# Kernel tuning notes

Hardware: AMD Instinct MI355X
Metric: run time of the kernel (lower is better)

The kernel has to match this reference:

```python
import jax, jax.numpy as jnp
import numpy as np

N_POINTS, N_TYPES, PER_TYPE, HIST, IN_U, U = 32768, 4, 8192, 32, 128, 128

def setup_inputs() -> dict:
    key = jax.random.key(0)
    ks = jax.random.split(key, 8)
    return {
        "current_node_state": jax.random.normal(ks[0], (N_POINTS, IN_U), jnp.float32),
        "historical_buffer": jax.random.normal(ks[1], (N_POINTS, HIST, U), jnp.float32),
        "entity_idx": jax.random.randint(ks[2], (N_TYPES, PER_TYPE), 0, N_POINTS, jnp.int32),
        "q_w": jax.random.normal(ks[3], (N_TYPES, IN_U, U), jnp.float32),
        "k_w": jax.random.normal(ks[4], (N_TYPES, U, U), jnp.float32),
        "v_w": jax.random.normal(ks[5], (N_TYPES, U, U), jnp.float32),
        "fc_w": jax.random.normal(ks[6], (N_TYPES, U, U), jnp.float32),
    }

def reference(current_node_state, historical_buffer, entity_idx, q_w, k_w, v_w, fc_w):
    # Batched-by-type gather (the original Python loop over entity types,
    # vectorized since all types have equal counts here).
    x = current_node_state[entity_idx]        # (T, N, IN_U)
    h = historical_buffer[entity_idx]         # (T, N, H, U)
    q = jnp.einsum('tne,teu->tnu', x, q_w)[:, :, None, :]   # (T, N, 1, U)
    k = jnp.einsum('tnhu,tuv->tnhv', h, k_w)                # (T, N, H, U)
    v = jnp.einsum('tnhu,tuv->tnhv', h, v_w)                # (T, N, H, U)
    raw = jnp.einsum('tnou,tnhu->tnoh', q, k)               # (T, N, 1, H)
    # NOTE: original uses F.softmax(raw_score) with implicit dim; for a 3D
    # tensor torch's legacy rule picks dim=0 (the per-type entity axis).
    attn = jax.nn.softmax(raw, axis=1)                      # softmax over N within each type
    agg = jnp.einsum('tnoh,tnhu->tnou', attn, v)            # (T, N, 1, U)
    out = jax.nn.relu(jnp.einsum('tnou,tuv->tnov', agg, fc_w)) + q
    # cat over types along node dim, then final squeeze -> (n_points, U)
    return out.reshape(N_TYPES * PER_TYPE, U)
```

## Files before the change

### kernel.cpp

```cpp
#include <hip/hip_runtime.h>
#include <math.h>

#define NPTS 32768
#define NTYPES 4
#define PER_TYPE 8192
#define HIST 32
#define UD 128
#define XT_STRIDE 68


__device__ __forceinline__ unsigned fkey(float x) {
    unsigned b = __float_as_uint(x);
    return (b & 0x80000000u) ? ~b : (b | 0x80000000u);
}
__device__ __forceinline__ float funkey(unsigned k) {
    unsigned b = (k & 0x80000000u) ? (k & 0x7fffffffu) : ~k;
    return __uint_as_float(b);
}

__global__ __launch_bounds__(128) void prep_kernel(
    const float* __restrict__ k_w, const float* __restrict__ v_w,
    const float* __restrict__ fc_w, float* __restrict__ kT,
    float* __restrict__ wvf, unsigned* __restrict__ Mbits, float* __restrict__ S)
{
    int r = blockIdx.x;
    int t = blockIdx.y;
    int u = threadIdx.x;
    kT[(t * UD + r) * UD + u] = k_w[(t * UD + u) * UD + r];
    float acc = 0.f;
    const float* vrow = v_w + (t * UD + r) * UD;
    const float* fb = fc_w + t * UD * UD;
    #pragma unroll 8
    for (int m = 0; m < UD; ++m)
        acc = fmaf(vrow[m], fb[m * UD + u], acc);
    wvf[(t * UD + r) * UD + u] = acc;
    if (r == 0 && t == 0) { Mbits[u] = 0u; S[u] = 0.f; }
}

__global__ __launch_bounds__(256) void qqk_kernel(
    const float* __restrict__ x, const int* __restrict__ idx,
    const float* __restrict__ q_w, const float* __restrict__ kT,
    float* __restrict__ q_out, float* __restrict__ qk_out)
{
    __shared__ float xT[UD * XT_STRIDE];
    __shared__ float qT[UD * XT_STRIDE];
    __shared__ int srow[64];
    int tx = threadIdx.x;
    int bn = blockIdx.x;
    int t  = blockIdx.y;
    int n0 = bn * 64;

    if (tx < 64) srow[tx] = idx[t * PER_TYPE + n0 + tx];
    __syncthreads();

    {
        int e = tx & 127;
        int half = tx >> 7;
        for (int i = 0; i < 32; ++i) {
            int ent = half * 32 + i;
            xT[e * XT_STRIDE + ent] = x[(size_t)srow[ent] * UD + e];
        }
    }
    __syncthreads();

    const int c4 = (tx & 31) * 4;
    const int eg = tx >> 5;
    float acc[8][4];

    #pragma unroll
    for (int i = 0; i < 8; ++i)
        #pragma unroll
        for (int j = 0; j < 4; ++j) acc[i][j] = 0.f;
    {
        const float* qw = q_w + t * UD * UD;
        for (int e = 0; e < UD; ++e) {
            float4 w = *(const float4*)(qw + e * UD + c4);
            const float* xr = &xT[e * XT_STRIDE + eg * 8];
            float4 a0 = *(const float4*)(xr);
            float4 a1 = *(const float4*)(xr + 4);
            float av[8] = {a0.x, a0.y, a0.z, a0.w, a1.x, a1.y, a1.z, a1.w};
            #pragma unroll
            for (int i = 0; i < 8; ++i) {
                acc[i][0] = fmaf(av[i], w.x, acc[i][0]);
                acc[i][1] = fmaf(av[i], w.y, acc[i][1]);
                acc[i][2] = fmaf(av[i], w.z, acc[i][2]);
                acc[i][3] = fmaf(av[i], w.w, acc[i][3]);
            }
        }
    }
    #pragma unroll
    for (int i = 0; i < 8; ++i) {
        int g = t * PER_TYPE + n0 + eg * 8 + i;
        *(float4*)(q_out + (size_t)g * UD + c4) =
            make_float4(acc[i][0], acc[i][1], acc[i][2], acc[i][3]);
    }
    #pragma unroll
    for (int j = 0; j < 4; ++j) {
        float4 lo = make_float4(acc[0][j], acc[1][j], acc[2][j], acc[3][j]);
        float4 hi = make_float4(acc[4][j], acc[5][j], acc[6][j], acc[7][j]);
        *(float4*)(&qT[(c4 + j) * XT_STRIDE + eg * 8]) = lo;
        *(float4*)(&qT[(c4 + j) * XT_STRIDE + eg * 8 + 4]) = hi;
    }
    __syncthreads();

    #pragma unroll
    for (int i = 0; i < 8; ++i)
        #pragma unroll
        for (int j = 0; j < 4; ++j) acc[i][j] = 0.f;
    {
        const float* kw = kT + t * UD * UD;
        for (int v = 0; v < UD; ++v) {
            float4 w = *(const float4*)(kw + v * UD + c4);
            const float* qr = &qT[v * XT_STRIDE + eg * 8];
            float4 a0 = *(const float4*)(qr);
            float4 a1 = *(const float4*)(qr + 4);
            float av[8] = {a0.x, a0.y, a0.z, a0.w, a1.x, a1.y, a1.z, a1.w};
            #pragma unroll
            for (int i = 0; i < 8; ++i) {
                acc[i][0] = fmaf(av[i], w.x, acc[i][0]);
                acc[i][1] = fmaf(av[i], w.y, acc[i][1]);
                acc[i][2] = fmaf(av[i], w.z, acc[i][2]);
                acc[i][3] = fmaf(av[i], w.w, acc[i][3]);
            }
        }
    }
    #pragma unroll
    for (int i = 0; i < 8; ++i) {
        int g = t * PER_TYPE + n0 + eg * 8 + i;
        *(float4*)(qk_out + (size_t)g * UD + c4) =
            make_float4(acc[i][0], acc[i][1], acc[i][2], acc[i][3]);
    }
}

__global__ __launch_bounds__(256) void raw_kernel(
    const float* __restrict__ hist, const int* __restrict__ idx,
    const float* __restrict__ qk, float* __restrict__ raw,
    unsigned* __restrict__ Mbits)
{
    __shared__ int srow[32];
    int tx = threadIdx.x;
    int bn = blockIdx.x;
    int t  = blockIdx.y;
    int n0 = bn * 32;
    if (tx < 32) srow[tx] = idx[t * PER_TYPE + n0 + tx];
    __syncthreads();
    int sub = tx & 7;
    int hh  = tx >> 3;
    float vmax = -INFINITY;
    for (int ei = 0; ei < 32; ++ei) {
        int g = t * PER_TYPE + n0 + ei;
        const float* qr = qk + (size_t)g * UD + sub * 16;
        float4 q0 = *(const float4*)(qr);
        float4 q1 = *(const float4*)(qr + 4);
        float4 q2 = *(const float4*)(qr + 8);
        float4 q3 = *(const float4*)(qr + 12);
        const float* hr = hist + ((size_t)srow[ei] * HIST + hh) * UD + sub * 16;
        float4 h0 = *(const float4*)(hr);
        float4 h1 = *(const float4*)(hr + 4);
        float4 h2 = *(const float4*)(hr + 8);
        float4 h3 = *(const float4*)(hr + 12);
        float a = q0.x * h0.x + q0.y * h0.y + q0.z * h0.z + q0.w * h0.w;
        a = fmaf(q1.x, h1.x, fmaf(q1.y, h1.y, fmaf(q1.z, h1.z, fmaf(q1.w, h1.w, a))));
        a = fmaf(q2.x, h2.x, fmaf(q2.y, h2.y, fmaf(q2.z, h2.z, fmaf(q2.w, h2.w, a))));
        a = fmaf(q3.x, h3.x, fmaf(q3.y, h3.y, fmaf(q3.z, h3.z, fmaf(q3.w, h3.w, a))));
        a += __shfl_xor(a, 1);
        a += __shfl_xor(a, 2);
        a += __shfl_xor(a, 4);
        vmax = fmaxf(vmax, a);
        if (sub == 0) raw[(size_t)g * HIST + hh] = a;
    }
    if (sub == 0) atomicMax(&Mbits[t * HIST + hh], fkey(vmax));
}

__global__ __launch_bounds__(256) void sum_kernel(
    const float* __restrict__ raw, const unsigned* __restrict__ Mbits,
    float* __restrict__ S)
{
    __shared__ float red[8][32];
    int tx = threadIdx.x;
    int c = blockIdx.x;
    int t = blockIdx.y;
    int hh = tx & 31;
    int nsl = tx >> 5;
    float M = funkey(Mbits[t * HIST + hh]);
    float s = 0.f;
    for (int i = 0; i < 32; ++i) {
        int n = c * 256 + i * 8 + nsl;
        float r = raw[((size_t)t * PER_TYPE + n) * HIST + hh];
        float e = r - M;
        if (e > -85.f) s += expf(e);
    }
    red[nsl][hh] = s;
    __syncthreads();
    if (tx < 32) {
        float tot = 0.f;
        #pragma unroll
        for (int k = 0; k < 8; ++k) tot += red[k][tx];
        atomicAdd(&S[t * HIST + tx], tot);
    }
}

__global__ __launch_bounds__(256) void out_kernel(
    const float* __restrict__ hist, const int* __restrict__ idx,
    const float* __restrict__ q, const float* __restrict__ raw,
    const unsigned* __restrict__ Mbits, const float* __restrict__ S,
    const float* __restrict__ wvf, float* __restrict__ out)
{
    __shared__ float shbar[4][UD];
    int tx = threadIdx.x;
    int wave = tx >> 6;
    int lane = tx & 63;
    int g = blockIdx.x * 4 + wave;
    int t = g >> 13;
    float w = 0.f;
    if (lane < 32) {
        float r = raw[(size_t)g * HIST + lane];
        float M = funkey(Mbits[t * HIST + lane]);
        float e = r - M;
        if (e > -75.f) w = expf(e) / S[t * HIST + lane];
    }
    unsigned long long act = __ballot(w != 0.f);
    int u2 = lane * 2;
    float2 qv = *(const float2*)(q + (size_t)g * UD + u2);
    float2 o;
    if (act == 0ull) {
        o = qv;
    } else {
        int row = idx[g];
        float2 hb = make_float2(0.f, 0.f);
        unsigned long long m = act;
        while (m) {
            int hh = __ffsll(m) - 1;
            m &= m - 1;
            float wv = __shfl(w, hh);
            float2 hv = *(const float2*)(hist + ((size_t)row * HIST + hh) * UD + u2);
            hb.x = fmaf(wv, hv.x, hb.x);
            hb.y = fmaf(wv, hv.y, hb.y);
        }
        shbar[wave][u2] = hb.x;
        shbar[wave][u2 + 1] = hb.y;
        float2 a = make_float2(0.f, 0.f);
        const float* wt = wvf + t * UD * UD;
        for (int e = 0; e < UD; ++e) {
            float hbe = shbar[wave][e];
            float2 wr = *(const float2*)(wt + e * UD + u2);
            a.x = fmaf(hbe, wr.x, a.x);
            a.y = fmaf(hbe, wr.y, a.y);
        }
        o.x = fmaxf(a.x, 0.f) + qv.x;
        o.y = fmaxf(a.y, 0.f) + qv.y;
    }
    *(float2*)(out + (size_t)g * UD + u2) = o;
}

extern "C" void kernel_launch(void* const* d_in, const int* in_sizes, int n_in,
                              void* d_out, int out_size, void* d_ws, size_t ws_size,
                              hipStream_t stream) {
    const float* x    = (const float*)d_in[0];
    const float* hist = (const float*)d_in[1];
    const int*   idx  = (const int*)d_in[2];
    const float* q_w  = (const float*)d_in[3];
    const float* k_w  = (const float*)d_in[4];
    const float* v_w  = (const float*)d_in[5];
    const float* fc_w = (const float*)d_in[6];
    float* out = (float*)d_out;

    float* ws = (float*)d_ws;
    float* q     = ws;
    float* qk    = ws + 4194304;
    float* raw   = ws + 8388608;
    unsigned* Mb = (unsigned*)(ws + 9437184);
    float* S     = ws + 9437312;
    float* kT    = ws + 9437440;
    float* wvf   = ws + 9502976;

    prep_kernel<<<dim3(128, 4), 128, 0, stream>>>(k_w, v_w, fc_w, kT, wvf, Mb, S);
    qqk_kernel<<<dim3(128, 4), 256, 0, stream>>>(x, idx, q_w, kT, q, qk);
    raw_kernel<<<dim3(256, 4), 256, 0, stream>>>(hist, idx, qk, raw, Mb);
    sum_kernel<<<dim3(32, 4), 256, 0, stream>>>(raw, Mb, S);
    out_kernel<<<8192, 256, 0, stream>>>(hist, idx, q, raw, Mb, S, wvf, out);
}
```

Measured before the change: 747.9 us.

## Restructure raw_kernel: stage qk in LDS, wider per-thread loads, block-level max

Raw-score kernel now handles 16 entities per block (twice as many blocks) and stages each entity's qk row in shared memory instead of re-reading it from global memory per thread group. Each thread covers 32 elements of the history row with 8 float4 loads and uses four independent partial sums, which needs one fewer shuffle step. The per-column max is reduced in shared memory before one global atomic per column per block, cutting global atomic traffic. The cost is extra LDS use, more registers per thread and a second block barrier.

```diff
diff --git a/kernel.cpp b/kernel.cpp
--- a/kernel.cpp
+++ b/kernel.cpp
@@ -137,39 +137,68 @@
     const float* __restrict__ qk, float* __restrict__ raw,
     unsigned* __restrict__ Mbits)
 {
-    __shared__ int srow[32];
+    __shared__ int srow[16];
+    __shared__ float sqk[16 * UD];
+    __shared__ unsigned smax[HIST];
     int tx = threadIdx.x;
     int bn = blockIdx.x;
     int t  = blockIdx.y;
-    int n0 = bn * 32;
-    if (tx < 32) srow[tx] = idx[t * PER_TYPE + n0 + tx];
-    __syncthreads();
-    int sub = tx & 7;
-    int hh  = tx >> 3;
+    int n0 = bn * 16;
+    if (tx < 16) srow[tx] = idx[t * PER_TYPE + n0 + tx];
+    if (tx < HIST) smax[tx] = 0u;
+    {
+        int e = tx >> 4;
+        int c = (tx & 15) * 8;
+        const float* src = qk + ((size_t)(t * PER_TYPE + n0 + e)) * UD + c;
+        float4 a = *(const float4*)(src);
+        float4 b = *(const float4*)(src + 4);
+        *(float4*)(&sqk[e * UD + c]) = a;
+        *(float4*)(&sqk[e * UD + c + 4]) = b;
+    }
+    __syncthreads();
+
+    int sub = tx & 3;
+    int hh  = (tx >> 2) & 31;
+    int eh  = tx >> 7;
     float vmax = -INFINITY;
-    for (int ei = 0; ei < 32; ++ei) {
-        int g = t * PER_TYPE + n0 + ei;
-        const float* qr = qk + (size_t)g * UD + sub * 16;
+    for (int j = 0; j < 8; ++j) {
+        int ei = j * 2 + eh;
+        int g  = t * PER_TYPE + n0 + ei;
+        const float* hr = hist + ((size_t)srow[ei] * HIST + hh) * UD + sub * 32;
+        float4 h0 = *(const float4*)(hr);
+        float4 h1 = *(const float4*)(hr + 4);
+        float4 h2 = *(const float4*)(hr + 8);
+        float4 h3 = *(const float4*)(hr + 12);
+        float4 h4 = *(const float4*)(hr + 16);
+        float4 h5 = *(const float4*)(hr + 20);
+        float4 h6 = *(const float4*)(hr + 24);
+        float4 h7 = *(const float4*)(hr + 28);
+        const float* qr = &sqk[ei * UD + sub * 32];
         float4 q0 = *(const float4*)(qr);
         float4 q1 = *(const float4*)(qr + 4);
         float4 q2 = *(const float4*)(qr + 8);
         float4 q3 = *(const float4*)(qr + 12);
-        const float* hr = hist + ((size_t)srow[ei] * HIST + hh) * UD + sub * 16;
-        float4 h0 = *(const float4*)(hr);
-        float4 h1 = *(const float4*)(hr + 4);
-        float4 h2 = *(const float4*)(hr + 8);
-        float4 h3 = *(const float4*)(hr + 12);
-        float a = q0.x * h0.x + q0.y * h0.y + q0.z * h0.z + q0.w * h0.w;
-        a = fmaf(q1.x, h1.x, fmaf(q1.y, h1.y, fmaf(q1.z, h1.z, fmaf(q1.w, h1.w, a))));
-        a = fmaf(q2.x, h2.x, fmaf(q2.y, h2.y, fmaf(q2.z, h2.z, fmaf(q2.w, h2.w, a))));
-        a = fmaf(q3.x, h3.x, fmaf(q3.y, h3.y, fmaf(q3.z, h3.z, fmaf(q3.w, h3.w, a))));
+        float4 q4 = *(const float4*)(qr + 16);
+        float4 q5 = *(const float4*)(qr + 20);
+        float4 q6 = *(const float4*)(qr + 24);
+        float4 q7 = *(const float4*)(qr + 28);
+        float p0 = q0.x * h0.x + q0.y * h0.y + q0.z * h0.z + q0.w * h0.w;
+        float p1 = q1.x * h1.x + q1.y * h1.y + q1.z * h1.z + q1.w * h1.w;
+        float p2 = q2.x * h2.x + q2.y * h2.y + q2.z * h2.z + q2.w * h2.w;
+        float p3 = q3.x * h3.x + q3.y * h3.y + q3.z * h3.z + q3.w * h3.w;
+        p0 = fmaf(q4.x, h4.x, fmaf(q4.y, h4.y, fmaf(q4.z, h4.z, fmaf(q4.w, h4.w, p0))));
+        p1 = fmaf(q5.x, h5.x, fmaf(q5.y, h5.y, fmaf(q5.z, h5.z, fmaf(q5.w, h5.w, p1))));
+        p2 = fmaf(q6.x, h6.x, fmaf(q6.y, h6.y, fmaf(q6.z, h6.z, fmaf(q6.w, h6.w, p2))));
+        p3 = fmaf(q7.x, h7.x, fmaf(q7.y, h7.y, fmaf(q7.z, h7.z, fmaf(q7.w, h7.w, p3))));
+        float a = (p0 + p1) + (p2 + p3);
         a += __shfl_xor(a, 1);
         a += __shfl_xor(a, 2);
-        a += __shfl_xor(a, 4);
         vmax = fmaxf(vmax, a);
         if (sub == 0) raw[(size_t)g * HIST + hh] = a;
     }
-    if (sub == 0) atomicMax(&Mbits[t * HIST + hh], fkey(vmax));
+    if (sub == 0) atomicMax(&smax[hh], fkey(vmax));
+    __syncthreads();
+    if (tx < HIST) atomicMax(&Mbits[t * HIST + tx], smax[tx]);
 }
 
 __global__ __launch_bounds__(256) void sum_kernel(
@@ -276,7 +305,7 @@
 
     prep_kernel<<<dim3(128, 4), 128, 0, stream>>>(k_w, v_w, fc_w, kT, wvf, Mb, S);
     qqk_kernel<<<dim3(128, 4), 256, 0, stream>>>(x, idx, q_w, kT, q, qk);
-    raw_kernel<<<dim3(256, 4), 256, 0, stream>>>(hist, idx, qk, raw, Mb);
+    raw_kernel<<<dim3(512, 4), 256, 0, stream>>>(hist, idx, qk, raw, Mb);
     sum_kernel<<<dim3(32, 4), 256, 0, stream>>>(raw, Mb, S);
     out_kernel<<<8192, 256, 0, stream>>>(hist, idx, q, raw, Mb, S, wvf, out);
 }
```

Measured after the change: 747.1 us. No clear change (-0.1%).
